# Kernel optimization log

Measured on AMD Instinct MI355X. Metric: run time of the kernel, lower is better.

The kernel has to match this reference:

```python
import jax, jax.numpy as jnp
import numpy as np

N = 40000      # nodes
E = 640000     # edges
F_IN = 128     # features_channels
H = 512        # GraphConv hidden
G = 64         # graphs in batch


def _glorot(key, shape):
    fan_in, fan_out = shape
    lim = float(np.sqrt(6.0 / (fan_in + fan_out)))
    return jax.random.uniform(key, shape, jnp.float32, -lim, lim)


def setup_inputs() -> dict:
    key = jax.random.key(0)
    ks = jax.random.split(key, 16)
    x = jax.random.normal(ks[0], (N, F_IN), jnp.float32)
    edge_index = jax.random.randint(ks[1], (2, E), 0, N, jnp.int64)
    edge_attr = jax.random.uniform(ks[2], (E,), jnp.float32)
    batch = jnp.sort(jax.random.randint(ks[3], (N,), 0, G, jnp.int64))
    return {
        "x": x, "edge_index": edge_index, "edge_attr": edge_attr, "batch": batch,
        # GraphConv1: lin_rel (with bias) on aggregated msgs, lin_root (no bias) on x
        "W_rel1": _glorot(ks[4], (F_IN, H)), "b_rel1": jnp.zeros((H,), jnp.float32),
        "W_root1": _glorot(ks[5], (F_IN, H)),
        "W_rel2": _glorot(ks[6], (H, H)), "b_rel2": jnp.zeros((H,), jnp.float32),
        "W_root2": _glorot(ks[7], (H, H)),
        # dense head
        "W1": _glorot(ks[8], (H, 64)), "b1": jnp.zeros((64,), jnp.float32),
        "W2": _glorot(ks[9], (64, 16)), "b2": jnp.zeros((16,), jnp.float32),
        "W3": _glorot(ks[10], (16, 1)), "b3": jnp.zeros((1,), jnp.float32),
    }


def _graph_conv(x, src, dst, ew, W_rel, b_rel, W_root):
    # PyG GraphConv (aggr='add'): out = lin_rel(sum_{j->i} w_ij * x_j) + lin_root(x_i)
    msg = x[src] * ew[:, None]                              # [E, C]
    agg = jax.ops.segment_sum(msg, dst, num_segments=N)     # [N, C]
    return agg @ W_rel + b_rel + x @ W_root


def reference(x, edge_index, edge_attr, batch,
              W_rel1, b_rel1, W_root1, W_rel2, b_rel2, W_root2,
              W1, b1, W2, b2, W3, b3):
    src, dst = edge_index[0], edge_index[1]
    h = jax.nn.relu(_graph_conv(x, src, dst, edge_attr, W_rel1, b_rel1, W_root1))
    h = jax.nn.relu(_graph_conv(h, src, dst, edge_attr, W_rel2, b_rel2, W_root2))
    # global_mean_pool over graph ids
    sums = jax.ops.segment_sum(h, batch, num_segments=G)            # [G, H]
    cnts = jax.ops.segment_sum(jnp.ones((N,), h.dtype), batch, num_segments=G)
    pooled = sums / jnp.maximum(cnts, 1.0)[:, None]
    # dropout is identity in eval mode
    o = jax.nn.relu(pooled @ W1 + b1)
    o = jax.nn.relu(o @ W2 + b2)
    return o @ W3 + b3                                               # [G, 1]
```

## Files before the change

kernel.cpp:

```cpp
#include <hip/hip_runtime.h>
#include <hip/hip_bf16.h>

#define NNODES 40000
#define MPAD   40192
#define NEDGES 640000
#define FIN    128
#define HID    512
#define NGRAPH 64

typedef __attribute__((ext_vector_type(8))) short bf16x8;
typedef __attribute__((ext_vector_type(4))) float f32x4;

__device__ __forceinline__ unsigned short f2bf(float f) {
    unsigned int u = __builtin_bit_cast(unsigned int, f);
    u += 0x7FFFu + ((u >> 16) & 1u);
    return (unsigned short)(u >> 16);
}
__device__ __forceinline__ float bf2f(unsigned short s) {
    return __builtin_bit_cast(float, (unsigned int)s << 16);
}

__device__ __forceinline__ void gload_lds16(const void* g, void* l) {
    __builtin_amdgcn_global_load_lds(
        (const __attribute__((address_space(1))) void*)g,
        (__attribute__((address_space(3))) void*)l, 16, 0, 0);
}


__global__ void k_cvt_x(const float* __restrict__ x, unsigned short* __restrict__ xb) {
    size_t e = ((size_t)blockIdx.x * 256 + threadIdx.x) * 8;
    if (e >= (size_t)MPAD * FIN) return;
    bf16x8 o;
    if (e < (size_t)NNODES * FIN) {
        float4 v0 = *(const float4*)(x + e);
        float4 v1 = *(const float4*)(x + e + 4);
        o[0] = f2bf(v0.x); o[1] = f2bf(v0.y); o[2] = f2bf(v0.z); o[3] = f2bf(v0.w);
        o[4] = f2bf(v1.x); o[5] = f2bf(v1.y); o[6] = f2bf(v1.z); o[7] = f2bf(v1.w);
    } else {
        o = (bf16x8)0;
    }
    *(bf16x8*)(xb + e) = o;
}

__global__ void k_cvt_wt(const float* __restrict__ W, unsigned short* __restrict__ Wt, int K) {
    int t = blockIdx.x * 256 + threadIdx.x;
    if (t >= 512 * K) return;
    int n = t / K, k = t - n * K;
    Wt[t] = f2bf(W[(size_t)k * 512 + n]);
}


__global__ void k_deg(const int* __restrict__ dst, int* __restrict__ deg) {
    int e = blockIdx.x * 256 + threadIdx.x;
    if (e < NEDGES) atomicAdd(&deg[dst[e]], 1);
}

__global__ void k_scan(const int* __restrict__ deg, int* __restrict__ off, int* __restrict__ cursor) {
    __shared__ int sh[1024];
    constexpr int CH = (NNODES + 1023) / 1024;
    int t = threadIdx.x;
    int base = t * CH;
    int vals[CH];
    int local = 0;
#pragma unroll
    for (int i = 0; i < CH; ++i) {
        int idx = base + i;
        int v = (idx < NNODES) ? deg[idx] : 0;
        vals[i] = v;
        local += v;
    }
    sh[t] = local;
    __syncthreads();
    for (int o = 1; o < 1024; o <<= 1) {
        int add = (t >= o) ? sh[t - o] : 0;
        __syncthreads();
        sh[t] += add;
        __syncthreads();
    }
    int run = sh[t] - local;
#pragma unroll
    for (int i = 0; i < CH; ++i) {
        int idx = base + i;
        if (idx < NNODES) {
            off[idx] = run;
            cursor[idx] = run;
            run += vals[i];
        }
    }
    if (t == 1023) off[NNODES] = sh[1023];
}

__global__ void k_fill(const int* __restrict__ src, const int* __restrict__ dst,
                       const float* __restrict__ ew, int* __restrict__ cursor,
                       int* __restrict__ csrc, float* __restrict__ cw) {
    int e = blockIdx.x * 256 + threadIdx.x;
    if (e < NEDGES) {
        int p = atomicAdd(&cursor[dst[e]], 1);
        csrc[p] = src[e];
        cw[p] = ew[e];
    }
}


__global__ void k_agg128(const unsigned short* __restrict__ xb, const int* __restrict__ off,
                         const int* __restrict__ csrc, const float* __restrict__ cw,
                         unsigned short* __restrict__ out) {
    int node = blockIdx.x * 4 + (threadIdx.x >> 6);
    if (node >= NNODES) return;
    int lane = threadIdx.x & 63;
    float a0 = 0.f, a1 = 0.f;
    int s = off[node], e = off[node + 1];
    for (int k = s; k < e; ++k) {
        int j = csrc[k];
        float w = cw[k];
        unsigned int v = *(const unsigned int*)(xb + (size_t)j * FIN + lane * 2);
        a0 += w * bf2f((unsigned short)(v & 0xFFFF));
        a1 += w * bf2f((unsigned short)(v >> 16));
    }
    unsigned int o = (unsigned int)f2bf(a0) | ((unsigned int)f2bf(a1) << 16);
    *(unsigned int*)(out + (size_t)node * FIN + lane * 2) = o;
}

__global__ void k_agg512(const unsigned short* __restrict__ h, const int* __restrict__ off,
                         const int* __restrict__ csrc, const float* __restrict__ cw,
                         unsigned short* __restrict__ out) {
    int node = blockIdx.x * 4 + (threadIdx.x >> 6);
    if (node >= NNODES) return;
    int lane = threadIdx.x & 63;
    float acc[8] = {};
    int s = off[node], e = off[node + 1];
    for (int k = s; k < e; ++k) {
        int j = csrc[k];
        float w = cw[k];
        bf16x8 a = *(const bf16x8*)(h + (size_t)j * HID + lane * 8);
#pragma unroll
        for (int q = 0; q < 8; ++q)
            acc[q] += w * bf2f((unsigned short)a[q]);
    }
    bf16x8 o;
#pragma unroll
    for (int q = 0; q < 8; ++q) o[q] = (short)f2bf(acc[q]);
    *(bf16x8*)(out + (size_t)node * HID + lane * 8) = o;
}


template <int K, bool POOL>
__global__ __launch_bounds__(512, 2)
void k_mfma_dual(const unsigned short* __restrict__ A0, const unsigned short* __restrict__ B0t,
                 const unsigned short* __restrict__ A1, const unsigned short* __restrict__ B1t,
                 const float* __restrict__ bias,
                 unsigned short* __restrict__ C,
                 const int* __restrict__ batch, float* __restrict__ psum) {
    constexpr int KT = K / 32;
    constexpr int S = 2 * KT;
    __shared__ unsigned short As[4][256 * 32];
    __shared__ unsigned short Bs[4][256 * 32];
    int tid = threadIdx.x;
    int l = tid & 63, w = tid >> 6;
    int wr = w >> 2, wc = w & 3;
    int bid = blockIdx.x;
    int row0 = (bid >> 1) * 256;
    int col0 = (bid & 1) * 256;

    int lr = l & 15, hi = l >> 4;
    int pofs = (hi ^ ((lr >> 1) & 3)) * 8;

    const unsigned short* Amat[2] = {A0, A1};
    const unsigned short* Bmat[2] = {B0t, B1t};

    int c0 = tid, c1 = tid + 512;
    int r0 = c0 >> 2, g0 = (c0 & 3) ^ ((r0 >> 1) & 3);
    int r1 = c1 >> 2, g1 = (c1 & 3) ^ ((r1 >> 1) & 3);

    auto stage_half = [&](int s, int half) {
        int mat = s / KT;
        int k0 = (s - mat * KT) * 32;
        const unsigned short* A = Amat[mat];
        const unsigned short* Bt = Bmat[mat];
        int c = half ? c1 : c0;
        int r = half ? r1 : r0;
        int g = half ? g1 : g0;
        gload_lds16(A + (size_t)(row0 + r) * K + k0 + g * 8, &As[s & 3][c * 8]);
        gload_lds16(Bt + (size_t)(col0 + r) * K + k0 + g * 8, &Bs[s & 3][c * 8]);
    };

    f32x4 acc[8][4];
#pragma unroll
    for (int m = 0; m < 8; ++m)
#pragma unroll
        for (int n = 0; n < 4; ++n) acc[m][n] = (f32x4)0.f;

    stage_half(0, 0); stage_half(0, 1);
    stage_half(1, 0); stage_half(1, 1);
    asm volatile("s_waitcnt vmcnt(4)" ::: "memory");
    __builtin_amdgcn_s_barrier();

    for (int s = 0; s < S; ++s) {
        const unsigned short* Ab = &As[s & 3][0];
        const unsigned short* Bb = &Bs[s & 3][0];
        bf16x8 af0[4], af1[4], bfr[4];
#pragma unroll
        for (int m = 0; m < 4; ++m)
            af0[m] = *(const bf16x8*)&Ab[(wr * 128 + m * 16 + lr) * 32 + pofs];
#pragma unroll
        for (int n = 0; n < 4; ++n)
            bfr[n] = *(const bf16x8*)&Bb[(wc * 64 + n * 16 + lr) * 32 + pofs];
        if (s + 2 < S) stage_half(s + 2, 0);
        __builtin_amdgcn_s_setprio(1);
#pragma unroll
        for (int m = 0; m < 4; ++m)
#pragma unroll
            for (int n = 0; n < 4; ++n)
                acc[m][n] = __builtin_amdgcn_mfma_f32_16x16x32_bf16(af0[m], bfr[n], acc[m][n], 0, 0, 0);
        __builtin_amdgcn_s_setprio(0);
#pragma unroll
        for (int m = 0; m < 4; ++m)
            af1[m] = *(const bf16x8*)&Ab[(wr * 128 + (4 + m) * 16 + lr) * 32 + pofs];
        if (s + 2 < S) stage_half(s + 2, 1);
        __builtin_amdgcn_s_setprio(1);
#pragma unroll
        for (int m = 0; m < 4; ++m)
#pragma unroll
            for (int n = 0; n < 4; ++n)
                acc[4 + m][n] = __builtin_amdgcn_mfma_f32_16x16x32_bf16(af1[m], bfr[n], acc[4 + m][n], 0, 0, 0);
        __builtin_amdgcn_s_setprio(0);
        if (s + 2 < S) {
            asm volatile("s_waitcnt vmcnt(4)" ::: "memory");
        } else {
            asm volatile("s_waitcnt vmcnt(0)" ::: "memory");
        }
        if (s + 1 < S) __builtin_amdgcn_s_barrier();
    }

    float bv[4];
#pragma unroll
    for (int n = 0; n < 4; ++n) bv[n] = bias[col0 + wc * 64 + n * 16 + lr];
    int rbase = row0 + wr * 128 + hi * 4;

    if constexpr (!POOL) {
#pragma unroll
        for (int m = 0; m < 8; ++m) {
#pragma unroll
            for (int i = 0; i < 4; ++i) {
                int rr = rbase + m * 16 + i;
                if (rr < NNODES) {
#pragma unroll
                    for (int n = 0; n < 4; ++n) {
                        int col = col0 + wc * 64 + n * 16 + lr;
                        C[(size_t)rr * HID + col] = f2bf(fmaxf(acc[m][n][i] + bv[n], 0.f));
                    }
                }
            }
        }
    } else {
#pragma unroll
        for (int m = 0; m < 8; ++m) {
            int b[4];
#pragma unroll
            for (int i = 0; i < 4; ++i) {
                int rr = rbase + m * 16 + i;
                b[i] = (rr < NNODES) ? batch[rr] : -1;
            }
#pragma unroll
            for (int n = 0; n < 4; ++n) {
                int col = col0 + wc * 64 + n * 16 + lr;
                int cb = -1;
                float run = 0.f;
#pragma unroll
                for (int i = 0; i < 4; ++i) {
                    if (b[i] >= 0) {
                        float v = fmaxf(acc[m][n][i] + bv[n], 0.f);
                        if (b[i] == cb) {
                            run += v;
                        } else {
                            if (cb >= 0) atomicAdd(&psum[(size_t)cb * HID + col], run);
                            cb = b[i];
                            run = v;
                        }
                    }
                }
                if (cb >= 0) atomicAdd(&psum[(size_t)cb * HID + col], run);
            }
        }
    }
}


__global__ void k_cnt(const int* __restrict__ batch, float* __restrict__ cnt) {
    __shared__ int h[NGRAPH];
    int t = threadIdx.x;
    if (t < NGRAPH) h[t] = 0;
    __syncthreads();
    int i = blockIdx.x * 256 + t;
    if (i < NNODES) atomicAdd(&h[batch[i]], 1);
    __syncthreads();
    if (t < NGRAPH && h[t] != 0) atomicAdd(&cnt[t], (float)h[t]);
}

__global__ void k_head(const float* __restrict__ psum, const float* __restrict__ cnt,
                       const float* __restrict__ W1, const float* __restrict__ b1,
                       const float* __restrict__ W2, const float* __restrict__ b2,
                       const float* __restrict__ W3, const float* __restrict__ b3,
                       float* __restrict__ out) {
    __shared__ float pooled[HID];
    __shared__ float o1[64];
    __shared__ float o2[16];
    int g = blockIdx.x, t = threadIdx.x;
    float c = fmaxf(cnt[g], 1.0f);
    for (int k = t; k < HID; k += 64) pooled[k] = psum[(size_t)g * HID + k] / c;
    __syncthreads();
    float a = b1[t];
    for (int k = 0; k < HID; ++k) a += pooled[k] * W1[k * 64 + t];
    o1[t] = fmaxf(a, 0.f);
    __syncthreads();
    if (t < 16) {
        float a2 = b2[t];
        for (int k = 0; k < 64; ++k) a2 += o1[k] * W2[k * 16 + t];
        o2[t] = fmaxf(a2, 0.f);
    }
    __syncthreads();
    if (t == 0) {
        float a3 = b3[0];
        for (int k = 0; k < 16; ++k) a3 += o2[k] * W3[k];
        out[g] = a3;
    }
}


extern "C" void kernel_launch(void* const* d_in, const int* in_sizes, int n_in,
                              void* d_out, int out_size, void* d_ws, size_t ws_size,
                              hipStream_t stream) {
    const float* x = (const float*)d_in[0];
    const int* ei = (const int*)d_in[1];
    const int* src = ei;
    const int* dst = ei + NEDGES;
    const float* ew = (const float*)d_in[2];
    const int* batch = (const int*)d_in[3];
    const float* Wr1 = (const float*)d_in[4];
    const float* br1 = (const float*)d_in[5];
    const float* Wo1 = (const float*)d_in[6];
    const float* Wr2 = (const float*)d_in[7];
    const float* br2 = (const float*)d_in[8];
    const float* Wo2 = (const float*)d_in[9];
    const float* W1 = (const float*)d_in[10];
    const float* b1 = (const float*)d_in[11];
    const float* W2 = (const float*)d_in[12];
    const float* b2 = (const float*)d_in[13];
    const float* W3 = (const float*)d_in[14];
    const float* b3 = (const float*)d_in[15];
    float* out = (float*)d_out;

    char* ws = (char*)d_ws;
    size_t o = 0;
    auto alloc = [&](size_t bytes) -> void* {
        void* p = ws + o;
        o = (o + bytes + 255) & ~(size_t)255;
        return p;
    };
    int* deg = (int*)alloc((size_t)NNODES * 4);
    int* off = (int*)alloc((size_t)(NNODES + 1) * 4);
    int* cur = (int*)alloc((size_t)NNODES * 4);
    int* csrc = (int*)alloc((size_t)NEDGES * 4);
    float* cw = (float*)alloc((size_t)NEDGES * 4);
    unsigned short* xb = (unsigned short*)alloc((size_t)MPAD * FIN * 2);
    unsigned short* agg1 = (unsigned short*)alloc((size_t)MPAD * FIN * 2);
    unsigned short* h1 = (unsigned short*)alloc((size_t)MPAD * HID * 2);
    unsigned short* agg2 = (unsigned short*)alloc((size_t)MPAD * HID * 2);
    unsigned short* Wr1t = (unsigned short*)alloc((size_t)512 * FIN * 2);
    unsigned short* Wo1t = (unsigned short*)alloc((size_t)512 * FIN * 2);
    unsigned short* Wr2t = (unsigned short*)alloc((size_t)512 * HID * 2);
    unsigned short* Wo2t = (unsigned short*)alloc((size_t)512 * HID * 2);
    float* psum = (float*)alloc((size_t)NGRAPH * HID * 4);
    float* cnt = (float*)alloc((size_t)NGRAPH * 4);

    hipMemsetAsync(deg, 0, (size_t)NNODES * 4, stream);
    hipMemsetAsync(psum, 0, (size_t)NGRAPH * HID * 4, stream);
    hipMemsetAsync(cnt, 0, (size_t)NGRAPH * 4, stream);

    k_cvt_x<<<((MPAD * FIN / 8) + 255) / 256, 256, 0, stream>>>(x, xb);
    k_cvt_wt<<<(512 * FIN + 255) / 256, 256, 0, stream>>>(Wr1, Wr1t, FIN);
    k_cvt_wt<<<(512 * FIN + 255) / 256, 256, 0, stream>>>(Wo1, Wo1t, FIN);
    k_cvt_wt<<<(512 * HID + 255) / 256, 256, 0, stream>>>(Wr2, Wr2t, HID);
    k_cvt_wt<<<(512 * HID + 255) / 256, 256, 0, stream>>>(Wo2, Wo2t, HID);

    k_deg<<<(NEDGES + 255) / 256, 256, 0, stream>>>(dst, deg);
    k_scan<<<1, 1024, 0, stream>>>(deg, off, cur);
    k_fill<<<(NEDGES + 255) / 256, 256, 0, stream>>>(src, dst, ew, cur, csrc, cw);

    k_agg128<<<(NNODES + 3) / 4, 256, 0, stream>>>(xb, off, csrc, cw, agg1);
    int nblk = (MPAD / 256) * 2;
    k_mfma_dual<FIN, false><<<nblk, 512, 0, stream>>>(agg1, Wr1t, xb, Wo1t, br1, h1, nullptr, nullptr);

    k_agg512<<<(NNODES + 3) / 4, 256, 0, stream>>>(h1, off, csrc, cw, agg2);
    k_cnt<<<(NNODES + 255) / 256, 256, 0, stream>>>(batch, cnt);
    k_mfma_dual<HID, true><<<nblk, 512, 0, stream>>>(agg2, Wr2t, h1, Wo2t, br2, nullptr, batch, psum);

    k_head<<<NGRAPH, 64, 0, stream>>>(psum, cnt, W1, b1, W2, b2, W3, b3, out);
}
```

Baseline: 467.3 us.

## Gather layer-2 neighbor features from an FP8 copy of h1

The first GEMM epilogue now writes an extra FP8 (e4m3) copy of the hidden activations, and the 512-wide aggregation kernel gathers from that copy instead of the bf16 one. This halves the bytes moved by the random-access neighbor gather, which is the bandwidth-bound step, at the cost of an extra byte-wise store in the epilogue and reduced precision in the aggregated messages. The MFMA main loop also issues both A-fragment LDS loads and both stage_half prefetches before the MFMAs, separated by a scheduling barrier.

Measured after the change: 453.1 us. 3.0% less time.

```diff
diff --git a/kernel.cpp b/kernel.cpp
--- a/kernel.cpp
+++ b/kernel.cpp
@@ -1,5 +1,6 @@
 #include <hip/hip_runtime.h>
 #include <hip/hip_bf16.h>
+#include <hip/hip_fp8.h>
 
 #define NNODES 40000
 #define MPAD   40192
@@ -10,6 +11,7 @@
 
 typedef __attribute__((ext_vector_type(8))) short bf16x8;
 typedef __attribute__((ext_vector_type(4))) float f32x4;
+typedef __attribute__((ext_vector_type(2))) float f32x2;
 
 __device__ __forceinline__ unsigned short f2bf(float f) {
     unsigned int u = __builtin_bit_cast(unsigned int, f);
@@ -18,6 +20,29 @@
 }
 __device__ __forceinline__ float bf2f(unsigned short s) {
     return __builtin_bit_cast(float, (unsigned int)s << 16);
+}
+
+__device__ __forceinline__ unsigned char f2fp8(float v) {
+#if __has_builtin(__builtin_amdgcn_cvt_pk_fp8_f32)
+    int p = __builtin_amdgcn_cvt_pk_fp8_f32(v, v, 0, false);
+    return (unsigned char)(p & 0xFF);
+#else
+    __hip_fp8_e4m3 q(v);
+    return (unsigned char)q.__x;
+#endif
+}
+template <bool HI>
+__device__ __forceinline__ f32x2 fp8pair2f(int word) {
+#if __has_builtin(__builtin_amdgcn_cvt_pk_f32_fp8)
+    return __builtin_amdgcn_cvt_pk_f32_fp8(word, HI);
+#else
+    f32x2 r;
+    __hip_fp8_e4m3 a, b;
+    a.__x = (unsigned char)((word >> (HI ? 16 : 0)) & 0xFF);
+    b.__x = (unsigned char)((word >> (HI ? 24 : 8)) & 0xFF);
+    r.x = (float)a; r.y = (float)b;
+    return r;
+#endif
 }
 
 __device__ __forceinline__ void gload_lds16(const void* g, void* l) {
@@ -121,7 +146,7 @@
     *(unsigned int*)(out + (size_t)node * FIN + lane * 2) = o;
 }
 
-__global__ void k_agg512(const unsigned short* __restrict__ h, const int* __restrict__ off,
+__global__ void k_agg512(const unsigned char* __restrict__ h8, const int* __restrict__ off,
                          const int* __restrict__ csrc, const float* __restrict__ cw,
                          unsigned short* __restrict__ out) {
     int node = blockIdx.x * 4 + (threadIdx.x >> 6);
@@ -132,10 +157,15 @@
     for (int k = s; k < e; ++k) {
         int j = csrc[k];
         float w = cw[k];
-        bf16x8 a = *(const bf16x8*)(h + (size_t)j * HID + lane * 8);
-#pragma unroll
-        for (int q = 0; q < 8; ++q)
-            acc[q] += w * bf2f((unsigned short)a[q]);
+        int2 v = *(const int2*)(h8 + (size_t)j * HID + lane * 8);
+        f32x2 f01 = fp8pair2f<false>(v.x);
+        f32x2 f23 = fp8pair2f<true>(v.x);
+        f32x2 f45 = fp8pair2f<false>(v.y);
+        f32x2 f67 = fp8pair2f<true>(v.y);
+        acc[0] += w * f01.x; acc[1] += w * f01.y;
+        acc[2] += w * f23.x; acc[3] += w * f23.y;
+        acc[4] += w * f45.x; acc[5] += w * f45.y;
+        acc[6] += w * f67.x; acc[7] += w * f67.y;
     }
     bf16x8 o;
 #pragma unroll
@@ -149,7 +179,7 @@
 void k_mfma_dual(const unsigned short* __restrict__ A0, const unsigned short* __restrict__ B0t,
                  const unsigned short* __restrict__ A1, const unsigned short* __restrict__ B1t,
                  const float* __restrict__ bias,
-                 unsigned short* __restrict__ C,
+                 unsigned short* __restrict__ C, unsigned char* __restrict__ C8,
                  const int* __restrict__ batch, float* __restrict__ psum) {
     constexpr int KT = K / 32;
     constexpr int S = 2 * KT;
@@ -203,9 +233,16 @@
         for (int m = 0; m < 4; ++m)
             af0[m] = *(const bf16x8*)&Ab[(wr * 128 + m * 16 + lr) * 32 + pofs];
 #pragma unroll
+        for (int m = 0; m < 4; ++m)
+            af1[m] = *(const bf16x8*)&Ab[(wr * 128 + (4 + m) * 16 + lr) * 32 + pofs];
+#pragma unroll
         for (int n = 0; n < 4; ++n)
             bfr[n] = *(const bf16x8*)&Bb[(wc * 64 + n * 16 + lr) * 32 + pofs];
-        if (s + 2 < S) stage_half(s + 2, 0);
+        if (s + 2 < S) {
+            stage_half(s + 2, 0);
+            stage_half(s + 2, 1);
+        }
+        __builtin_amdgcn_sched_barrier(0);
         __builtin_amdgcn_s_setprio(1);
 #pragma unroll
         for (int m = 0; m < 4; ++m)
@@ -213,10 +250,6 @@
             for (int n = 0; n < 4; ++n)
                 acc[m][n] = __builtin_amdgcn_mfma_f32_16x16x32_bf16(af0[m], bfr[n], acc[m][n], 0, 0, 0);
         __builtin_amdgcn_s_setprio(0);
-#pragma unroll
-        for (int m = 0; m < 4; ++m)
-            af1[m] = *(const bf16x8*)&Ab[(wr * 128 + (4 + m) * 16 + lr) * 32 + pofs];
-        if (s + 2 < S) stage_half(s + 2, 1);
         __builtin_amdgcn_s_setprio(1);
 #pragma unroll
         for (int m = 0; m < 4; ++m)
@@ -247,7 +280,9 @@
 #pragma unroll
                     for (int n = 0; n < 4; ++n) {
                         int col = col0 + wc * 64 + n * 16 + lr;
-                        C[(size_t)rr * HID + col] = f2bf(fmaxf(acc[m][n][i] + bv[n], 0.f));
+                        float v = fmaxf(acc[m][n][i] + bv[n], 0.f);
+                        C[(size_t)rr * HID + col] = f2bf(v);
+                        C8[(size_t)rr * HID + col] = f2fp8(v);
                     }
                 }
             }
@@ -365,6 +400,7 @@
     unsigned short* xb = (unsigned short*)alloc((size_t)MPAD * FIN * 2);
     unsigned short* agg1 = (unsigned short*)alloc((size_t)MPAD * FIN * 2);
     unsigned short* h1 = (unsigned short*)alloc((size_t)MPAD * HID * 2);
+    unsigned char* h1f8 = (unsigned char*)alloc((size_t)MPAD * HID);
     unsigned short* agg2 = (unsigned short*)alloc((size_t)MPAD * HID * 2);
     unsigned short* Wr1t = (unsigned short*)alloc((size_t)512 * FIN * 2);
     unsigned short* Wo1t = (unsigned short*)alloc((size_t)512 * FIN * 2);
@@ -389,11 +425,11 @@
 
     k_agg128<<<(NNODES + 3) / 4, 256, 0, stream>>>(xb, off, csrc, cw, agg1);
     int nblk = (MPAD / 256) * 2;
-    k_mfma_dual<FIN, false><<<nblk, 512, 0, stream>>>(agg1, Wr1t, xb, Wo1t, br1, h1, nullptr, nullptr);
-
-    k_agg512<<<(NNODES + 3) / 4, 256, 0, stream>>>(h1, off, csrc, cw, agg2);
+    k_mfma_dual<FIN, false><<<nblk, 512, 0, stream>>>(agg1, Wr1t, xb, Wo1t, br1, h1, h1f8, nullptr, nullptr);
+
+    k_agg512<<<(NNODES + 3) / 4, 256, 0, stream>>>(h1f8, off, csrc, cw, agg2);
     k_cnt<<<(NNODES + 255) / 256, 256, 0, stream>>>(batch, cnt);
-    k_mfma_dual<HID, true><<<nblk, 512, 0, stream>>>(agg2, Wr2t, h1, Wo2t, br2, nullptr, batch, psum);
+    k_mfma_dual<HID, true><<<nblk, 512, 0, stream>>>(agg2, Wr2t, h1, Wo2t, br2, nullptr, nullptr, batch, psum);
 
     k_head<<<NGRAPH, 64, 0, stream>>>(psum, cnt, W1, b1, W2, b2, W3, b3, out);
 }
```
